# Performance work log

Measured on AMD Instinct MI355X. Metric: run time of the kernel, lower is better.

The kernel has to match this reference:

```python
import jax, jax.numpy as jnp
import numpy as np

N_NODES = 10000


def _sage_conv(x, src, dst, W_l, W_r, b):
    # mean aggregation of source features at destination nodes (PyG SAGEConv default)
    msg = x[src]                                             # [E, C_in]
    agg = jax.ops.segment_sum(msg, dst, num_segments=N_NODES)  # [N, C_in]
    cnt = jax.ops.segment_sum(jnp.ones((src.shape[0],), x.dtype), dst,
                              num_segments=N_NODES)
    mean = agg / jnp.maximum(cnt, 1.0)[:, None]              # isolated nodes -> 0
    return mean @ W_l + x @ W_r + b


def setup_inputs() -> dict:
    key = jax.random.key(0)
    ks = jax.random.split(key, 8)
    E = 640000
    x = jax.random.normal(ks[0], (N_NODES, 128), dtype=jnp.float32)
    edge_index = jax.random.randint(ks[1], (2, E), 0, N_NODES, dtype=jnp.int64)
    W1_l = jax.random.normal(ks[2], (128, 256), dtype=jnp.float32) * 0.05
    W1_r = jax.random.normal(ks[3], (128, 256), dtype=jnp.float32) * 0.05
    b1 = jnp.zeros((256,), dtype=jnp.float32)
    W2_l = jax.random.normal(ks[4], (256, 128), dtype=jnp.float32) * 0.05
    W2_r = jax.random.normal(ks[5], (256, 128), dtype=jnp.float32) * 0.05
    b2 = jnp.zeros((128,), dtype=jnp.float32)
    return {"x": x, "edge_index": edge_index, "W1_l": W1_l, "W1_r": W1_r,
            "b1": b1, "W2_l": W2_l, "W2_r": W2_r, "b2": b2}


def reference(x, edge_index, W1_l, W1_r, b1, W2_l, W2_r, b2):
    src, dst = edge_index[0], edge_index[1]
    h = jax.nn.relu(_sage_conv(x, src, dst, W1_l, W1_r, b1))
    out = _sage_conv(h, src, dst, W2_l, W2_r, b2)
    return out
```

## Files before the change

kernel.cpp:

```cpp
#include <hip/hip_runtime.h>

#define N_NODES 10000
#define HB 64

typedef unsigned int uint;
typedef unsigned short ushort;
typedef __attribute__((ext_vector_type(8))) short bf16x8;
typedef __attribute__((ext_vector_type(4))) float f32x4;

__device__ __forceinline__ ushort f2bf(float f) {
    uint b = __float_as_uint(f);
    b += 0x7fffu + ((b >> 16) & 1u);
    return (ushort)(b >> 16);
}

#define CAST_B 1250
#define TCAST_B 512

__global__ __launch_bounds__(256) void prep_kernel(const float* __restrict__ x,
                                                   const float* __restrict__ W1l,
                                                   const float* __restrict__ W1r,
                                                   const float* __restrict__ W2l,
                                                   const float* __restrict__ W2r,
                                                   const int* __restrict__ dst, int E, int chunk,
                                                   int* __restrict__ chunk_hist,
                                                   ushort* __restrict__ lrank,
                                                   ushort* __restrict__ xb,
                                                   ushort* __restrict__ W1T,
                                                   ushort* __restrict__ W2T,
                                                   int* __restrict__ aggv) {
    __shared__ int hist[N_NODES];
    int b = blockIdx.x;
    int t = threadIdx.x;
    if (b < HB) {
        for (int i = t; i < N_NODES; i += 256) hist[i] = 0;
        __syncthreads();
        int e0 = b * chunk;
        int e1 = e0 + chunk; if (e1 > E) e1 = E;
        for (int e = e0 + t; e < e1; e += 256) {
            int d = dst[e];
            lrank[e] = (ushort)atomicAdd(&hist[d], 1);
        }
        __syncthreads();
        for (int i = t; i < N_NODES; i += 256) chunk_hist[b * N_NODES + i] = hist[i];
    } else if (b < HB + CAST_B) {
        if (b == HB && t < 64) aggv[t] = 0;
        int i = (b - HB) * 256 + t;
        float4 v = ((const float4*)x)[i];
        ushort4 o;
        o.x = f2bf(v.x); o.y = f2bf(v.y); o.z = f2bf(v.z); o.w = f2bf(v.w);
        ((ushort4*)xb)[i] = o;
    } else {
        int id = (b - HB - CAST_B) * 256 + t;
        int z = id >> 16;
        int k = (id >> 8) & 255;
        int c = id & 255;
        if (z == 0) {
            float v = (k < 128) ? W1l[k * 256 + c] : W1r[(k - 128) * 256 + c];
            W1T[c * 256 + k] = f2bf(v);
        } else {
            float v = (c < 128) ? W2l[k * 128 + c] : W2r[k * 128 + (c - 128)];
            W2T[c * 256 + k] = f2bf(v);
        }
    }
}

__global__ __launch_bounds__(256) void csr_mid_kernel(int* __restrict__ ch,
                                                      int* __restrict__ row_ptr,
                                                      int* __restrict__ aggv) {
    int b = blockIdx.x, t = threadIdx.x;
    int n = b * 256 + t;
    bool ok = n < N_NODES;
    int s = 0;
    if (ok) {
#pragma unroll 8
        for (int c = 0; c < HB; ++c) s += ch[c * N_NODES + n];
    }
    int lane = t & 63, wid = t >> 6;
    int incl = s;
#pragma unroll
    for (int off = 1; off < 64; off <<= 1) {
        int y = __shfl_up(incl, off);
        if (lane >= off) incl += y;
    }
    __shared__ int wsum[4];
    __shared__ int sbase;
    if (lane == 63) wsum[wid] = incl;
    __syncthreads();
    int tot = wsum[0] + wsum[1] + wsum[2] + wsum[3];
    int wbase = 0;
#pragma unroll
    for (int w = 0; w < 4; ++w)
        if (w < wid) wbase += wsum[w];
    incl += wbase;
    if (t == 0)
        __hip_atomic_store(&aggv[b], tot + 1, __ATOMIC_RELEASE, __HIP_MEMORY_SCOPE_AGENT);
    if (t < 64) {
        int v = 0;
        if (t < b) {
            do {
                v = __hip_atomic_load(&aggv[t], __ATOMIC_ACQUIRE, __HIP_MEMORY_SCOPE_AGENT);
            } while (v == 0);
            --v;
        }
#pragma unroll
        for (int m = 1; m < 64; m <<= 1) v += __shfl_xor(v, m);
        if (t == 0) sbase = v;
    }
    __syncthreads();
    int base = sbase;
    if (b == 0 && t == 0) row_ptr[0] = 0;
    if (ok) {
        row_ptr[n + 1] = base + incl;
        int run = base + incl - s;
#pragma unroll 8
        for (int c = 0; c < HB; ++c) {
            int v = ch[c * N_NODES + n];
            ch[c * N_NODES + n] = run;
            run += v;
        }
    }
}

__global__ __launch_bounds__(256) void scatter_kernel(const int* __restrict__ src,
                                                      const int* __restrict__ dst,
                                                      const ushort* __restrict__ lrank,
                                                      const int* __restrict__ off,
                                                      int E, int chunk,
                                                      ushort* __restrict__ csr) {
    int g = blockIdx.x * blockDim.x + threadIdx.x;
    int e = g * 4;
    if (e + 3 < E) {
        int b = e / chunk;
        const int* ob = off + b * N_NODES;
        int4 d = *(const int4*)&dst[e];
        int4 s = *(const int4*)&src[e];
        ushort4 r = *(const ushort4*)&lrank[e];
        csr[ob[d.x] + r.x] = (ushort)s.x;
        csr[ob[d.y] + r.y] = (ushort)s.y;
        csr[ob[d.z] + r.z] = (ushort)s.z;
        csr[ob[d.w] + r.w] = (ushort)s.w;
    } else {
        for (; e < E; ++e)
            csr[off[(e / chunk) * N_NODES + dst[e]] + lrank[e]] = (ushort)src[e];
    }
}

template <int MODE>
__global__ __launch_bounds__(256) void agg_kernel(const ushort* __restrict__ feat,
                                                  const int* __restrict__ row_ptr,
                                                  const ushort* __restrict__ csr,
                                                  uint* __restrict__ outb,
                                                  float* __restrict__ out) {
    int wave = threadIdx.x >> 6;
    int lane = threadIdx.x & 63;
    int n = blockIdx.x * 4 + wave;
    if (n >= N_NODES) return;
    int beg = row_ptr[n], end = row_ptr[n + 1];
    const uint* f = (const uint*)feat;
    float ax0 = 0, ay0 = 0, ax1 = 0, ay1 = 0, ax2 = 0, ay2 = 0, ax3 = 0, ay3 = 0;
    int i = beg;
    for (; i + 4 <= end; i += 4) {
        int s0 = csr[i + 0];
        int s1 = csr[i + 1];
        int s2 = csr[i + 2];
        int s3 = csr[i + 3];
        uint u0 = f[s0 * 64 + lane];
        uint u1 = f[s1 * 64 + lane];
        uint u2 = f[s2 * 64 + lane];
        uint u3 = f[s3 * 64 + lane];
        ax0 += __uint_as_float(u0 << 16); ay0 += __uint_as_float(u0 & 0xffff0000u);
        ax1 += __uint_as_float(u1 << 16); ay1 += __uint_as_float(u1 & 0xffff0000u);
        ax2 += __uint_as_float(u2 << 16); ay2 += __uint_as_float(u2 & 0xffff0000u);
        ax3 += __uint_as_float(u3 << 16); ay3 += __uint_as_float(u3 & 0xffff0000u);
    }
    for (; i < end; ++i) {
        int s = csr[i];
        uint u = f[s * 64 + lane];
        ax0 += __uint_as_float(u << 16); ay0 += __uint_as_float(u & 0xffff0000u);
    }
    float deg = (float)(end - beg);
    float inv = deg > 0.f ? 1.0f / deg : 0.0f;
    float sx = ((ax0 + ax1) + (ax2 + ax3)) * inv;
    float sy = ((ay0 + ay1) + (ay2 + ay3)) * inv;
    if (MODE == 0) {
        outb[n * 64 + lane] = (uint)f2bf(sx) | ((uint)f2bf(sy) << 16);
    } else {
        float2* o = (float2*)&out[n * 128 + lane * 2];
        float2 prev = *o;
        prev.x += sx; prev.y += sy;
        *o = prev;
    }
}

__global__ __launch_bounds__(256) void gemm_fused(const ushort* __restrict__ m1b,
                                                  const ushort* __restrict__ xb,
                                                  const ushort* __restrict__ W1T,
                                                  const float* __restrict__ b1,
                                                  const ushort* __restrict__ W2T,
                                                  const float* __restrict__ b2,
                                                  ushort* __restrict__ t,
                                                  float* __restrict__ out) {
    __shared__ ushort hsh[16 * 264];
    int w = threadIdx.x >> 6, lane = threadIdx.x & 63;
    int lr = lane & 15, lg = lane >> 4;
    int r0 = blockIdx.x * 16;
    int row = r0 + lr;
    int c0 = w * 64;

    bf16x8 afr[8];
#pragma unroll
    for (int ks = 0; ks < 8; ++ks) {
        int k0 = ks * 32;
        const ushort* Ab = (k0 < 128) ? (m1b + row * 128 + k0) : (xb + row * 128 + (k0 - 128));
        afr[ks] = *(const bf16x8*)(Ab + lg * 8);
    }

    {
        f32x4 acc[4] = {};
#pragma unroll
        for (int ks = 0; ks < 8; ++ks) {
            int k0 = ks * 32;
#pragma unroll
            for (int cg = 0; cg < 4; ++cg) {
                int col = c0 + cg * 16 + lr;
                bf16x8 b = *(const bf16x8*)(W1T + col * 256 + k0 + lg * 8);
                acc[cg] = __builtin_amdgcn_mfma_f32_16x16x32_bf16(afr[ks], b, acc[cg], 0, 0, 0);
            }
        }
#pragma unroll
        for (int cg = 0; cg < 4; ++cg) {
            int col = c0 + cg * 16 + lr;
            float bias = b1[col];
#pragma unroll
            for (int i = 0; i < 4; ++i) {
                float v = acc[cg][i] + bias;
                v = v > 0.f ? v : 0.f;
                hsh[(lg * 4 + i) * 264 + col] = f2bf(v);
            }
        }
    }
    __syncthreads();

    bf16x8 afr2[8];
#pragma unroll
    for (int ks = 0; ks < 8; ++ks)
        afr2[ks] = *(const bf16x8*)&hsh[lr * 264 + ks * 32 + lg * 8];

    {
        f32x4 acc[4] = {};
#pragma unroll
        for (int ks = 0; ks < 8; ++ks) {
            int k0 = ks * 32;
#pragma unroll
            for (int cg = 0; cg < 4; ++cg) {
                int col = c0 + cg * 16 + lr;
                bf16x8 b = *(const bf16x8*)(W2T + col * 256 + k0 + lg * 8);
                acc[cg] = __builtin_amdgcn_mfma_f32_16x16x32_bf16(afr2[ks], b, acc[cg], 0, 0, 0);
            }
        }
#pragma unroll
        for (int cg = 0; cg < 4; ++cg) {
            int col = c0 + cg * 16 + lr;
            if (col < 128) {
#pragma unroll
                for (int i = 0; i < 4; ++i)
                    t[(r0 + lg * 4 + i) * 128 + col] = f2bf(acc[cg][i]);
            } else {
                int oc = col - 128;
                float bias = b2[oc];
#pragma unroll
                for (int i = 0; i < 4; ++i)
                    out[(r0 + lg * 4 + i) * 128 + oc] = acc[cg][i] + bias;
            }
        }
    }
}


extern "C" void kernel_launch(void* const* d_in, const int* in_sizes, int n_in,
                              void* d_out, int out_size, void* d_ws, size_t ws_size,
                              hipStream_t stream) {
    const float* x   = (const float*)d_in[0];
    const int* edge  = (const int*)d_in[1];
    const float* W1l = (const float*)d_in[2];
    const float* W1r = (const float*)d_in[3];
    const float* b1  = (const float*)d_in[4];
    const float* W2l = (const float*)d_in[5];
    const float* W2r = (const float*)d_in[6];
    const float* b2  = (const float*)d_in[7];
    float* out = (float*)d_out;

    int E = in_sizes[1] / 2;
    const int* src = edge;
    const int* dst = edge + E;
    int chunk = (((E + HB - 1) / HB) + 3) & ~3;

    ushort* m1b  = (ushort*)d_ws;
    ushort* hb   = m1b + (size_t)N_NODES * 128;
    ushort* xb   = hb + (size_t)N_NODES * 256;
    ushort* W1T  = xb + (size_t)N_NODES * 128;
    ushort* W2T  = W1T + 256 * 256;
    ushort* csr  = W2T + 256 * 256;
    ushort* lrank= csr + E;
    int* chist   = (int*)(lrank + E);
    int* row_ptr = chist + HB * N_NODES;
    int* aggv    = row_ptr + (N_NODES + 1);
    ushort* tb   = m1b;

    prep_kernel<<<HB + CAST_B + TCAST_B, 256, 0, stream>>>(x, W1l, W1r, W2l, W2r,
                                                           dst, E, chunk, chist, lrank,
                                                           xb, W1T, W2T, aggv);

    csr_mid_kernel<<<(N_NODES + 255) / 256, 256, 0, stream>>>(chist, row_ptr, aggv);

    scatter_kernel<<<(E / 4 + 255) / 256, 256, 0, stream>>>(src, dst, lrank, chist, E, chunk, csr);

    agg_kernel<0><<<(N_NODES + 3) / 4, 256, 0, stream>>>(xb, row_ptr, csr, (uint*)m1b, nullptr);

    gemm_fused<<<N_NODES / 16, 256, 0, stream>>>(m1b, xb, W1T, b1, W2T, b2, tb, out);

    agg_kernel<1><<<(N_NODES + 3) / 4, 256, 0, stream>>>(tb, row_ptr, csr, nullptr, out);
}
```

Before: 107.7 us.

## Fuse CSR offset scan and edge scatter into one kernel with flag sync

Merges the row-pointer/offset scan kernel and the edge scatter kernel into a single launch. The scatter blocks preload their edge data and then spin on per-block completion flags written by the scan blocks. This removes one kernel launch and the gap between the two kernels. It depends on the scan blocks being scheduled before or alongside the scatter blocks, which lower block indices normally are. Separately, the aggregation loop is unrolled to 8 neighbours per iteration so more gathers are in flight at once.

```diff
diff --git a/kernel.cpp b/kernel.cpp
--- a/kernel.cpp
+++ b/kernel.cpp
@@ -2,6 +2,7 @@
 
 #define N_NODES 10000
 #define HB 64
+#define NMID 40
 
 typedef unsigned int uint;
 typedef unsigned short ushort;
@@ -44,7 +45,7 @@
         __syncthreads();
         for (int i = t; i < N_NODES; i += 256) chunk_hist[b * N_NODES + i] = hist[i];
     } else if (b < HB + CAST_B) {
-        if (b == HB && t < 64) aggv[t] = 0;
+        if (b == HB && t < 128) aggv[t] = 0;
         int i = (b - HB) * 256 + t;
         float4 v = ((const float4*)x)[i];
         ushort4 o;
@@ -65,84 +66,99 @@
     }
 }
 
-__global__ __launch_bounds__(256) void csr_mid_kernel(int* __restrict__ ch,
-                                                      int* __restrict__ row_ptr,
-                                                      int* __restrict__ aggv) {
+__global__ __launch_bounds__(256, 4) void csr_finish(const int* __restrict__ src,
+                                                     const int* __restrict__ dst,
+                                                     const ushort* __restrict__ lrank,
+                                                     int* __restrict__ ch,
+                                                     int* __restrict__ row_ptr,
+                                                     int* __restrict__ aggv,
+                                                     int* __restrict__ offsdone,
+                                                     int E, int chunk,
+                                                     ushort* __restrict__ csr) {
     int b = blockIdx.x, t = threadIdx.x;
-    int n = b * 256 + t;
-    bool ok = n < N_NODES;
-    int s = 0;
-    if (ok) {
+    if (b < NMID) {
+        int n = b * 256 + t;
+        bool ok = n < N_NODES;
+        int s = 0;
+        if (ok) {
 #pragma unroll 8
-        for (int c = 0; c < HB; ++c) s += ch[c * N_NODES + n];
-    }
-    int lane = t & 63, wid = t >> 6;
-    int incl = s;
-#pragma unroll
-    for (int off = 1; off < 64; off <<= 1) {
-        int y = __shfl_up(incl, off);
-        if (lane >= off) incl += y;
-    }
-    __shared__ int wsum[4];
-    __shared__ int sbase;
-    if (lane == 63) wsum[wid] = incl;
-    __syncthreads();
-    int tot = wsum[0] + wsum[1] + wsum[2] + wsum[3];
-    int wbase = 0;
-#pragma unroll
-    for (int w = 0; w < 4; ++w)
-        if (w < wid) wbase += wsum[w];
-    incl += wbase;
-    if (t == 0)
-        __hip_atomic_store(&aggv[b], tot + 1, __ATOMIC_RELEASE, __HIP_MEMORY_SCOPE_AGENT);
-    if (t < 64) {
-        int v = 0;
-        if (t < b) {
-            do {
-                v = __hip_atomic_load(&aggv[t], __ATOMIC_ACQUIRE, __HIP_MEMORY_SCOPE_AGENT);
-            } while (v == 0);
-            --v;
-        }
-#pragma unroll
-        for (int m = 1; m < 64; m <<= 1) v += __shfl_xor(v, m);
-        if (t == 0) sbase = v;
-    }
-    __syncthreads();
-    int base = sbase;
-    if (b == 0 && t == 0) row_ptr[0] = 0;
-    if (ok) {
-        row_ptr[n + 1] = base + incl;
-        int run = base + incl - s;
+            for (int c = 0; c < HB; ++c) s += ch[c * N_NODES + n];
+        }
+        int lane = t & 63, wid = t >> 6;
+        int incl = s;
+#pragma unroll
+        for (int off = 1; off < 64; off <<= 1) {
+            int y = __shfl_up(incl, off);
+            if (lane >= off) incl += y;
+        }
+        __shared__ int wsum[4];
+        __shared__ int sbase;
+        if (lane == 63) wsum[wid] = incl;
+        __syncthreads();
+        int tot = wsum[0] + wsum[1] + wsum[2] + wsum[3];
+        int wbase = 0;
+#pragma unroll
+        for (int w = 0; w < 4; ++w)
+            if (w < wid) wbase += wsum[w];
+        incl += wbase;
+        if (t == 0)
+            __hip_atomic_store(&aggv[b], tot + 1, __ATOMIC_RELEASE, __HIP_MEMORY_SCOPE_AGENT);
+        if (t < 64) {
+            int v = 0;
+            if (t < b) {
+                do {
+                    v = __hip_atomic_load(&aggv[t], __ATOMIC_ACQUIRE, __HIP_MEMORY_SCOPE_AGENT);
+                } while (v == 0);
+                --v;
+            }
+#pragma unroll
+            for (int m = 1; m < 64; m <<= 1) v += __shfl_xor(v, m);
+            if (t == 0) sbase = v;
+        }
+        __syncthreads();
+        int base = sbase;
+        if (b == 0 && t == 0) row_ptr[0] = 0;
+        if (ok) {
+            row_ptr[n + 1] = base + incl;
+            int run = base + incl - s;
 #pragma unroll 8
-        for (int c = 0; c < HB; ++c) {
-            int v = ch[c * N_NODES + n];
-            ch[c * N_NODES + n] = run;
-            run += v;
-        }
-    }
-}
-
-__global__ __launch_bounds__(256) void scatter_kernel(const int* __restrict__ src,
-                                                      const int* __restrict__ dst,
-                                                      const ushort* __restrict__ lrank,
-                                                      const int* __restrict__ off,
-                                                      int E, int chunk,
-                                                      ushort* __restrict__ csr) {
-    int g = blockIdx.x * blockDim.x + threadIdx.x;
-    int e = g * 4;
-    if (e + 3 < E) {
-        int b = e / chunk;
-        const int* ob = off + b * N_NODES;
-        int4 d = *(const int4*)&dst[e];
-        int4 s = *(const int4*)&src[e];
-        ushort4 r = *(const ushort4*)&lrank[e];
-        csr[ob[d.x] + r.x] = (ushort)s.x;
-        csr[ob[d.y] + r.y] = (ushort)s.y;
-        csr[ob[d.z] + r.z] = (ushort)s.z;
-        csr[ob[d.w] + r.w] = (ushort)s.w;
+            for (int c = 0; c < HB; ++c) {
+                int v = ch[c * N_NODES + n];
+                ch[c * N_NODES + n] = run;
+                run += v;
+            }
+        }
+        __syncthreads();
+        if (t == 0)
+            __hip_atomic_store(&offsdone[b], 1, __ATOMIC_RELEASE, __HIP_MEMORY_SCOPE_AGENT);
     } else {
-        for (; e < E; ++e)
-            csr[off[(e / chunk) * N_NODES + dst[e]] + lrank[e]] = (ushort)src[e];
+        int g = (b - NMID) * 256 + t;
+        int e = g * 4;
+        bool full = (e + 3 < E);
+        int4 d, sv; ushort4 r;
+        if (full) {
+            d = *(const int4*)&dst[e];
+            sv = *(const int4*)&src[e];
+            r = *(const ushort4*)&lrank[e];
+        }
+        if (t < NMID) {
+            while (__hip_atomic_load(&offsdone[t], __ATOMIC_ACQUIRE,
+                                     __HIP_MEMORY_SCOPE_AGENT) == 0)
+                __builtin_amdgcn_s_sleep(8);
+        }
+        __syncthreads();
+        __builtin_amdgcn_fence(__ATOMIC_ACQUIRE, "agent");
+        if (full) {
+            int bb = e / chunk;
+            const int* ob = ch + bb * N_NODES;
+            csr[ob[d.x] + r.x] = (ushort)sv.x;
+            csr[ob[d.y] + r.y] = (ushort)sv.y;
+            csr[ob[d.z] + r.z] = (ushort)sv.z;
+            csr[ob[d.w] + r.w] = (ushort)sv.w;
+        } else {
+            for (; e < E; ++e)
+                csr[ch[(e / chunk) * N_NODES + dst[e]] + lrank[e]] = (ushort)src[e];
+        }
     }
 }
 
@@ -160,6 +176,32 @@
     const uint* f = (const uint*)feat;
     float ax0 = 0, ay0 = 0, ax1 = 0, ay1 = 0, ax2 = 0, ay2 = 0, ax3 = 0, ay3 = 0;
     int i = beg;
+    for (; i + 8 <= end; i += 8) {
+        int s0 = csr[i + 0];
+        int s1 = csr[i + 1];
+        int s2 = csr[i + 2];
+        int s3 = csr[i + 3];
+        int s4 = csr[i + 4];
+        int s5 = csr[i + 5];
+        int s6 = csr[i + 6];
+        int s7 = csr[i + 7];
+        uint u0 = f[s0 * 64 + lane];
+        uint u1 = f[s1 * 64 + lane];
+        uint u2 = f[s2 * 64 + lane];
+        uint u3 = f[s3 * 64 + lane];
+        uint u4 = f[s4 * 64 + lane];
+        uint u5 = f[s5 * 64 + lane];
+        uint u6 = f[s6 * 64 + lane];
+        uint u7 = f[s7 * 64 + lane];
+        ax0 += __uint_as_float(u0 << 16); ay0 += __uint_as_float(u0 & 0xffff0000u);
+        ax1 += __uint_as_float(u1 << 16); ay1 += __uint_as_float(u1 & 0xffff0000u);
+        ax2 += __uint_as_float(u2 << 16); ay2 += __uint_as_float(u2 & 0xffff0000u);
+        ax3 += __uint_as_float(u3 << 16); ay3 += __uint_as_float(u3 & 0xffff0000u);
+        ax0 += __uint_as_float(u4 << 16); ay0 += __uint_as_float(u4 & 0xffff0000u);
+        ax1 += __uint_as_float(u5 << 16); ay1 += __uint_as_float(u5 & 0xffff0000u);
+        ax2 += __uint_as_float(u6 << 16); ay2 += __uint_as_float(u6 & 0xffff0000u);
+        ax3 += __uint_as_float(u7 << 16); ay3 += __uint_as_float(u7 & 0xffff0000u);
+    }
     for (; i + 4 <= end; i += 4) {
         int s0 = csr[i + 0];
         int s1 = csr[i + 1];
@@ -306,15 +348,16 @@
     int* chist   = (int*)(lrank + E);
     int* row_ptr = chist + HB * N_NODES;
     int* aggv    = row_ptr + (N_NODES + 1);
+    int* offsdone= aggv + 64;
     ushort* tb   = m1b;
 
     prep_kernel<<<HB + CAST_B + TCAST_B, 256, 0, stream>>>(x, W1l, W1r, W2l, W2r,
                                                            dst, E, chunk, chist, lrank,
                                                            xb, W1T, W2T, aggv);
 
-    csr_mid_kernel<<<(N_NODES + 255) / 256, 256, 0, stream>>>(chist, row_ptr, aggv);
-
-    scatter_kernel<<<(E / 4 + 255) / 256, 256, 0, stream>>>(src, dst, lrank, chist, E, chunk, csr);
+    int nsc = (E / 4 + 255) / 256;
+    csr_finish<<<NMID + nsc, 256, 0, stream>>>(src, dst, lrank, chist, row_ptr,
+                                               aggv, offsdone, E, chunk, csr);
 
     agg_kernel<0><<<(N_NODES + 3) / 4, 256, 0, stream>>>(xb, row_ptr, csr, (uint*)m1b, nullptr);
 
```

Result: slower. 225.6 us (+109.4%).
